# Kernel tuning notes

Hardware: AMD Instinct MI355X
Metric: run time of the kernel (lower is better)

The kernel has to match this reference:

```python
import jax, jax.numpy as jnp
import numpy as np

R = 29          # GF_kernel_size_train
EPS = 1e-09     # loss_eps
SAMPLING = 8    # sampling_in_MSEloss
LAMBDA_TV = 0.1
LAMBDA_HESSIAN = 0.5
ISO = True      # isotropic_hessian
SIGMA = 1.0     # hessian_kernel_sigma (>0.5 -> generateHessianKernel, angle_offset=[0])


def _hessian_kernels():
    half = int(np.ceil(SIGMA * 6))
    t = np.linspace(-half, half, 2 * half + 1)
    X, Y = np.meshgrid(t, t, indexing='ij')
    g = np.exp(-(X ** 2 + Y ** 2) / (2 * SIGMA ** 2))
    dxx = (1.0 / (2 * np.pi * SIGMA ** 4)) * (X ** 2 / SIGMA ** 2 - 1) * g
    dxy = (1.0 / (2 * np.pi * SIGMA ** 6)) * (X * Y) * g
    dyy = dxx.T
    # Loss.__init__ unpacks generateHessianKernel's return (Gaussyy, Gaussxx, Gaussxy)
    # into (self.DGaussxx, self.DGaussyy, self.DGaussxy); angle_offset=[0] -> identity rotate.
    Gxx = dyy.astype(np.float32)[None, None]
    Gyy = dxx.astype(np.float32)[None, None]
    Gxy = dxy.astype(np.float32)[None, None]
    return jnp.asarray(Gxx), jnp.asarray(Gyy), jnp.asarray(Gxy)


def _conv(x, k):
    return jax.lax.conv_general_dilated(x, k, (1, 1), 'VALID',
                                        dimension_numbers=('NCHW', 'OIHW', 'NCHW'))


def _boxfilter(x, r):
    # F.pad(input, (r+1, r, r+1, r)) pads last two dims (left r+1, right r each)
    xp = jnp.pad(x, ((0, 0), (0, 0), (r + 1, r), (r + 1, r)))
    c = jnp.cumsum(xp, axis=3)
    d = c[:, :, :, 2 * r + 1:] - c[:, :, :, :-2 * r - 1]
    c2 = jnp.cumsum(d, axis=2)
    return c2[:, :, 2 * r + 1:, :] - c2[:, :, :-2 * r - 1, :]


def _guided_filter(x, y, r, eps):
    N = _boxfilter(jnp.ones_like(x), r)
    mean_x = _boxfilter(x, r) / N
    mean_y = _boxfilter(y, r) / N
    cov_xy = _boxfilter(x * y, r) / N - mean_x * mean_y
    var_x = _boxfilter(x * x, r) / N - mean_x * mean_x
    A = cov_xy / jnp.clip(var_x, EPS, None)
    b = mean_y - A * mean_x
    A = _boxfilter(A, r) / N
    b = _boxfilter(b, r) / N
    return A * x + b


def _tv(x, target, Dx, Dy):
    return jnp.abs(_conv(x, Dx)).sum() + jnp.abs(_conv(x - target, Dy)).sum()


def _hessian(x, target, Gxx, Gyy, Gxy):
    scale = 2.0 if ISO else 1.0
    return (jnp.abs(_conv(x, Gxx)).sum()
            + jnp.abs(_conv(x - target, Gyy)).sum()
            + (jnp.abs(_conv(x - target, Gxy)) * scale).sum())


def setup_inputs() -> dict:
    key = jax.random.key(0)
    ks = jax.random.split(key, 6)
    shape = (1, 1, 3072, 3072)
    Gxx, Gyy, Gxy = _hessian_kernels()
    return {
        'outputGNNraw': jax.random.normal(ks[0], shape, dtype=jnp.float32),
        'outputGNN': jax.random.normal(ks[1], shape, dtype=jnp.float32),
        'outputLR': jax.random.normal(ks[2], shape, dtype=jnp.float32),
        'smoothedTarget': jax.random.normal(ks[3], shape, dtype=jnp.float32),
        'targets': jax.random.normal(ks[4], shape, dtype=jnp.float32),
        'map': jax.random.uniform(ks[5], shape, dtype=jnp.float32),
        'Dx': jnp.array([[1.0, -1.0]], dtype=jnp.float32)[None, None],   # [1,1,1,2]
        'Dy': jnp.array([[1.0], [-1.0]], dtype=jnp.float32)[None, None], # [1,1,2,1]
        'DGaussxx': Gxx, 'DGaussyy': Gyy, 'DGaussxy': Gxy,
    }


def reference(outputGNNraw, outputGNN, outputLR, smoothedTarget, targets, map,
              Dx, Dy, DGaussxx, DGaussyy, DGaussxy):
    gf = _guided_filter(outputGNNraw, outputGNNraw, R, EPS)
    mse = (jnp.abs(smoothedTarget - gf).sum()
           + (jnp.abs(targets - outputGNN) * map)[:, :, ::SAMPLING, ::SAMPLING].sum())
    tv = _tv(outputGNN, targets, Dx, Dy) + _tv(outputLR, targets, Dx, Dy)
    hess = (_hessian(outputGNN, targets, DGaussxx, DGaussyy, DGaussxy)
            + _hessian(outputLR, targets, DGaussxx, DGaussyy, DGaussxy))
    return mse + LAMBDA_TV * tv + LAMBDA_HESSIAN * hess
```

## Files before the change

### kernel.cpp

```cpp
#include <hip/hip_runtime.h>
#include <math.h>

#define W    3072
#define HH   3072
#define HOUT 3060
#define TW   64
#define TH   44
#define RW   11
#define XR   56
#define XTS  76
#define VTS  77
#define VTW  (RW*VTS)
#define GX   48
#define GY   70
#define GZ   2
#define NBLK (GX*GY*GZ)
#define NTHR (NBLK*256)
#define NSLOT 64
#define NSTG ((XR*19+255)/256)

struct HessTaps { float a[13]; float bb[13]; float m[13]; float n[13]; };

__device__ double g_slots[NSLOT * 32];

__global__ __launch_bounds__(256, 5) void hess_kernel(const float* __restrict__ Gnn,
                                                      const float* __restrict__ Lr,
                                                      const float* __restrict__ T,
                                                      const float* __restrict__ Xr,
                                                      const float* __restrict__ St,
                                                      const float* __restrict__ Mp,
                                                      HessTaps tp) {
  __shared__ float xt[XR * XTS];
  __shared__ float vt[4 * VTW];
  __shared__ float red[4][3];
  const float* img = (blockIdx.z == 0) ? Gnn : Lr;
  int oy = blockIdx.y * TH, ox = blockIdx.x * TW;
  int t = threadIdx.x;
  int wv = t >> 6, ln = t & 63;
  int r0 = wv * RW;

  for (int idx = t; idx < XR * 19; idx += 256) {
    int r = idx / 19, g = idx - r * 19;
    int gr = oy + r, gc = ox + 4 * g;
    float4 v = {0.f, 0.f, 0.f, 0.f};
    if (gr < HH) {
      const float* p = &img[(size_t)gr * W + gc];
      if (gc + 3 < W) v = *(const float4*)p;
      else {
        if (gc < W)     v.x = p[0];
        if (gc + 1 < W) v.y = p[1];
        if (gc + 2 < W) v.z = p[2];
      }
    }
    *(float4*)&xt[r * XTS + 4 * g] = v;
  }

  float4 tr4[NSTG];
  #pragma unroll
  for (int k = 0; k < NSTG; ++k) {
    int idx = t + 256 * k;
    float4 v = {0.f, 0.f, 0.f, 0.f};
    if (idx < XR * 19) {
      int r = idx / 19, g = idx - r * 19;
      int gr = oy + r, gc = ox + 4 * g;
      if (gr < HH) {
        const float* p = &T[(size_t)gr * W + gc];
        if (gc + 3 < W) v = *(const float4*)p;
        else {
          if (gc < W)     v.x = p[0];
          if (gc + 1 < W) v.y = p[1];
          if (gc + 2 < W) v.z = p[2];
        }
      }
    }
    tr4[k] = v;
  }

  int bid = (blockIdx.z * GY + blockIdx.y) * GX + blockIdx.x;
  int i0 = bid * 256 + t;
  int i1 = i0 + NTHR;
  const int n4 = (W * HH) / 4;
  float4 ga0 = ((const float4*)Xr)[i0];
  float4 gb0 = ((const float4*)St)[i0];
  float4 ga1 = {0.f, 0.f, 0.f, 0.f}, gb1 = ga1;
  bool has1 = (i1 < n4);
  if (has1) { ga1 = ((const float4*)Xr)[i1]; gb1 = ((const float4*)St)[i1]; }
  float mT = 0.f, mG = 0.f, mM = 0.f;
  bool hasm = (i0 < 384 * 384);
  if (hasm) {
    int si = i0 / 384, sj = i0 - si * 384;
    int id = si * 8 * W + sj * 8;
    mT = T[id]; mG = Gnn[id]; mM = Mp[id];
  }
  __builtin_amdgcn_sched_barrier(0);

  __syncthreads();

  float tvl = 0.f;
  float hl  = 0.f;

  {
    int gc = ox + ln;
    if (gc < W - 1) {
      #pragma unroll
      for (int i = 0; i < RW; ++i) {
        int r = r0 + i;
        if (oy + r < HH)
          tvl += fabsf(xt[r * XTS + ln] - xt[r * XTS + ln + 1]);
      }
    }
  }

  #define VPASS(TAP)                                                        \
    {                                                                       \
       \
      float oA[RW];                                                         \
      _Pragma("unroll")                                                     \
      for (int i = 0; i < RW; ++i) oA[i] = 0.f;                             \
      _Pragma("unroll")                                                     \
      for (int u = 0; u < RW + 12; ++u) {                                   \
        float xA = xt[(r0 + u) * XTS + ln];                                 \
        _Pragma("unroll")                                                   \
        for (int i = 0; i < RW; ++i) {                                      \
          int kk = u - i;                                                   \
          if (kk >= 0 && kk <= 12) oA[i] = fmaf((TAP)[kk], xA, oA[i]);      \
        }                                                                   \
      }                                                                     \
      float* vw = &vt[wv * VTW + ln];                                       \
      _Pragma("unroll")                                                     \
      for (int i = 0; i < RW; ++i) vw[i * VTS] = oA[i];                     \
                   \
      _Pragma("unroll")                                                     \
      for (int k = 0; k < 3; ++k) {                                         \
        int o = ln + 64 * k;                                                \
        if (o < 12 * RW) {                                                  \
          int row = o / 12, hc = o - row * 12;                              \
          const float* xp = &xt[(r0 + row) * XTS + 64 + hc];                \
          float s = 0.f;                                                    \
          _Pragma("unroll")                                                 \
          for (int u = 0; u < 13; ++u) s = fmaf((TAP)[u], xp[u * XTS], s);  \
          vt[wv * VTW + row * VTS + 64 + hc] = s;                           \
        }                                                                   \
      }                                                                     \
    }

  #define HSECOND(TAP, WGT)                                                 \
    {                                                                       \
      int r14 = ln & 15, cg = ln >> 4;                                      \
      if (r14 < RW) {                                                       \
        const float* vrow = &vt[wv * VTW + r14 * VTS + cg * 16];            \
        float o_[16];                                                       \
        _Pragma("unroll")                                                   \
        for (int jj = 0; jj < 16; ++jj) o_[jj] = 0.f;                       \
        _Pragma("unroll")                                                   \
        for (int j = 0; j < 28; ++j) {                                      \
          float v = vrow[j];                                                \
          _Pragma("unroll")                                                 \
          for (int jj = 0; jj < 16; ++jj) {                                 \
            int kk = j - jj;                                                \
            if (kk >= 0 && kk <= 12) o_[jj] = fmaf((TAP)[kk], v, o_[jj]);   \
          }                                                                 \
        }                                                                   \
        int gr = oy + r0 + r14;                                             \
        int gc0 = ox + cg * 16;                                             \
        float wr = (gr < HOUT) ? (WGT) : 0.f;                               \
        _Pragma("unroll")                                                   \
        for (int jj = 0; jj < 16; ++jj) {                                   \
          float m_ = (gc0 + jj < HOUT) ? wr : 0.f;                          \
          hl = fmaf(m_, fabsf(o_[jj]), hl);                                 \
        }                                                                   \
      }                                                                     \
    }

  VPASS(tp.bb);
  HSECOND(tp.a, 1.0f);

  __syncthreads();
  #pragma unroll
  for (int k = 0; k < NSTG; ++k) {
    int idx = t + 256 * k;
    if (idx < XR * 19) {
      int r = idx / 19, g = idx - r * 19;
      float4 cur = *(float4*)&xt[r * XTS + 4 * g];
      cur.x -= tr4[k].x; cur.y -= tr4[k].y;
      cur.z -= tr4[k].z; cur.w -= tr4[k].w;
      *(float4*)&xt[r * XTS + 4 * g] = cur;
    }
  }
  __syncthreads();

  {
    int gc = ox + ln;
    if (gc < W) {
      #pragma unroll
      for (int i = 0; i < RW; ++i) {
        int r = r0 + i;
        if (oy + r < HH - 1)
          tvl += fabsf(xt[r * XTS + ln] - xt[(r + 1) * XTS + ln]);
      }
    }
  }

  VPASS(tp.a);
  HSECOND(tp.bb, 1.0f);

  VPASS(tp.m);
  HSECOND(tp.n, 2.0f);

  float gm = fabsf(gb0.x - ga0.x) + fabsf(gb0.y - ga0.y)
           + fabsf(gb0.z - ga0.z) + fabsf(gb0.w - ga0.w);
  if (has1)
    gm += fabsf(gb1.x - ga1.x) + fabsf(gb1.y - ga1.y)
        + fabsf(gb1.z - ga1.z) + fabsf(gb1.w - ga1.w);
  if (hasm) gm += fabsf(mT - mG) * mM;

  #pragma unroll
  for (int o = 32; o > 0; o >>= 1) {
    gm  += __shfl_down(gm,  o, 64);
    tvl += __shfl_down(tvl, o, 64);
    hl  += __shfl_down(hl,  o, 64);
  }
  if (ln == 0) { red[wv][0] = gm; red[wv][1] = tvl; red[wv][2] = hl; }
  __syncthreads();
  if (t == 0) {
    int slot = bid & (NSLOT - 1);
    double* base = g_slots + (size_t)slot * 32;
    unsafeAtomicAdd(base,      (double)(red[0][0] + red[1][0] + red[2][0] + red[3][0]));
    unsafeAtomicAdd(base + 8,  (double)(red[0][1] + red[1][1] + red[2][1] + red[3][1]));
    unsafeAtomicAdd(base + 16, (double)(red[0][2] + red[1][2] + red[2][2] + red[3][2]));
  }
}

__global__ __launch_bounds__(64) void finalize_kernel(float* __restrict__ out) {
  int t = threadIdx.x;
  double* b = g_slots + (size_t)t * 32;
  double s0 = b[0];  b[0]  = 0.0;
  double s1 = b[8];  b[8]  = 0.0;
  double s3 = b[16]; b[16] = 0.0;
  #pragma unroll
  for (int o = 32; o > 0; o >>= 1) {
    s0 += __shfl_down(s0, o, 64);
    s1 += __shfl_down(s1, o, 64);
    s3 += __shfl_down(s3, o, 64);
  }
  if (t == 0) out[0] = (float)(s0 + 0.1 * s1 + 0.5 * s3);
}

extern "C" void kernel_launch(void* const* d_in, const int* in_sizes, int n_in,
                              void* d_out, int out_size, void* d_ws, size_t ws_size,
                              hipStream_t stream) {
  const float* xraw = (const float*)d_in[0];
  const float* gnn  = (const float*)d_in[1];
  const float* lr   = (const float*)d_in[2];
  const float* st   = (const float*)d_in[3];
  const float* tg   = (const float*)d_in[4];
  const float* mp   = (const float*)d_in[5];
  float* out = (float*)d_out;

  HessTaps tp;
  const double PI2 = 6.283185307179586476925287;
  for (int k = 0; k < 13; ++k) {
    double tt = (double)(k - 6);
    double g = exp(-0.5 * tt * tt);
    tp.a[k]  = (float)((tt * tt - 1.0) * g / PI2);
    tp.bb[k] = (float)g;
    tp.m[k]  = (float)(tt * g / PI2);
    tp.n[k]  = (float)(tt * g);
  }

  hess_kernel<<<dim3(GX, GY, GZ), 256, 0, stream>>>(gnn, lr, tg, xraw, st, mp,
                                                    tp);
  finalize_kernel<<<1, 64, 0, stream>>>(out);
}
```

Before: 260.1 us.

## Retile hessian kernel to 512-thread blocks with taller tiles and smaller per-wave strips

Moves to 8 waves per block, each handling 7 rows, with a 56-row tile to cut vertical halo redundancy. The horizontal second pass is remapped to 8-column segments per lane, and the MSE stream now needs only one float4 per thread. The trade-off is idle lanes in the horizontal pass and a tight launch bound that may cause register spills.

```diff
diff --git a/kernel.cpp b/kernel.cpp
--- a/kernel.cpp
+++ b/kernel.cpp
@@ -5,25 +5,26 @@
 #define HH   3072
 #define HOUT 3060
 #define TW   64
-#define TH   44
-#define RW   11
-#define XR   56
+#define TH   56
+#define RW   7
+#define NW   8
+#define XR   68
 #define XTS  76
 #define VTS  77
 #define VTW  (RW*VTS)
 #define GX   48
-#define GY   70
+#define GY   55
 #define GZ   2
 #define NBLK (GX*GY*GZ)
-#define NTHR (NBLK*256)
+#define NTHR (NBLK*512)
 #define NSLOT 64
-#define NSTG ((XR*19+255)/256)
+#define NSTG ((XR*19+511)/512)
 
 struct HessTaps { float a[13]; float bb[13]; float m[13]; float n[13]; };
 
 __device__ double g_slots[NSLOT * 32];
 
-__global__ __launch_bounds__(256, 5) void hess_kernel(const float* __restrict__ Gnn,
+__global__ __launch_bounds__(512, 8) void hess_kernel(const float* __restrict__ Gnn,
                                                       const float* __restrict__ Lr,
                                                       const float* __restrict__ T,
                                                       const float* __restrict__ Xr,
@@ -31,15 +32,15 @@
                                                       const float* __restrict__ Mp,
                                                       HessTaps tp) {
   __shared__ float xt[XR * XTS];
-  __shared__ float vt[4 * VTW];
-  __shared__ float red[4][3];
+  __shared__ float vt[NW * VTW];
+  __shared__ float red[NW][3];
   const float* img = (blockIdx.z == 0) ? Gnn : Lr;
   int oy = blockIdx.y * TH, ox = blockIdx.x * TW;
   int t = threadIdx.x;
   int wv = t >> 6, ln = t & 63;
   int r0 = wv * RW;
 
-  for (int idx = t; idx < XR * 19; idx += 256) {
+  for (int idx = t; idx < XR * 19; idx += 512) {
     int r = idx / 19, g = idx - r * 19;
     int gr = oy + r, gc = ox + 4 * g;
     float4 v = {0.f, 0.f, 0.f, 0.f};
@@ -58,7 +59,7 @@
   float4 tr4[NSTG];
   #pragma unroll
   for (int k = 0; k < NSTG; ++k) {
-    int idx = t + 256 * k;
+    int idx = t + 512 * k;
     float4 v = {0.f, 0.f, 0.f, 0.f};
     if (idx < XR * 19) {
       int r = idx / 19, g = idx - r * 19;
@@ -77,14 +78,11 @@
   }
 
   int bid = (blockIdx.z * GY + blockIdx.y) * GX + blockIdx.x;
-  int i0 = bid * 256 + t;
-  int i1 = i0 + NTHR;
+  int i0 = bid * 512 + t;
   const int n4 = (W * HH) / 4;
-  float4 ga0 = ((const float4*)Xr)[i0];
-  float4 gb0 = ((const float4*)St)[i0];
-  float4 ga1 = {0.f, 0.f, 0.f, 0.f}, gb1 = ga1;
-  bool has1 = (i1 < n4);
-  if (has1) { ga1 = ((const float4*)Xr)[i1]; gb1 = ((const float4*)St)[i1]; }
+  float4 ga0 = {0.f, 0.f, 0.f, 0.f}, gb0 = ga0;
+  bool has0 = (i0 < n4);
+  if (has0) { ga0 = ((const float4*)Xr)[i0]; gb0 = ((const float4*)St)[i0]; }
   float mT = 0.f, mG = 0.f, mM = 0.f;
   bool hasm = (i0 < 384 * 384);
   if (hasm) {
@@ -113,7 +111,7 @@
 
   #define VPASS(TAP)                                                        \
     {                                                                       \
-       \
+        \
       float oA[RW];                                                         \
       _Pragma("unroll")                                                     \
       for (int i = 0; i < RW; ++i) oA[i] = 0.f;                             \
@@ -129,9 +127,9 @@
       float* vw = &vt[wv * VTW + ln];                                       \
       _Pragma("unroll")                                                     \
       for (int i = 0; i < RW; ++i) vw[i * VTS] = oA[i];                     \
-                   \
-      _Pragma("unroll")                                                     \
-      for (int k = 0; k < 3; ++k) {                                         \
+                     \
+      _Pragma("unroll")                                                     \
+      for (int k = 0; k < 2; ++k) {                                         \
         int o = ln + 64 * k;                                                \
         if (o < 12 * RW) {                                                  \
           int row = o / 12, hc = o - row * 12;                              \
@@ -146,26 +144,26 @@
 
   #define HSECOND(TAP, WGT)                                                 \
     {                                                                       \
-      int r14 = ln & 15, cg = ln >> 4;                                      \
-      if (r14 < RW) {                                                       \
-        const float* vrow = &vt[wv * VTW + r14 * VTS + cg * 16];            \
-        float o_[16];                                                       \
-        _Pragma("unroll")                                                   \
-        for (int jj = 0; jj < 16; ++jj) o_[jj] = 0.f;                       \
-        _Pragma("unroll")                                                   \
-        for (int j = 0; j < 28; ++j) {                                      \
+      int r8 = ln >> 3, cg = ln & 7;                                        \
+      if (r8 < RW) {                                                        \
+        const float* vrow = &vt[wv * VTW + r8 * VTS + cg * 8];              \
+        float o_[8];                                                        \
+        _Pragma("unroll")                                                   \
+        for (int jj = 0; jj < 8; ++jj) o_[jj] = 0.f;                        \
+        _Pragma("unroll")                                                   \
+        for (int j = 0; j < 20; ++j) {                                      \
           float v = vrow[j];                                                \
           _Pragma("unroll")                                                 \
-          for (int jj = 0; jj < 16; ++jj) {                                 \
+          for (int jj = 0; jj < 8; ++jj) {                                  \
             int kk = j - jj;                                                \
             if (kk >= 0 && kk <= 12) o_[jj] = fmaf((TAP)[kk], v, o_[jj]);   \
           }                                                                 \
         }                                                                   \
-        int gr = oy + r0 + r14;                                             \
-        int gc0 = ox + cg * 16;                                             \
+        int gr = oy + r0 + r8;                                              \
+        int gc0 = ox + cg * 8;                                              \
         float wr = (gr < HOUT) ? (WGT) : 0.f;                               \
         _Pragma("unroll")                                                   \
-        for (int jj = 0; jj < 16; ++jj) {                                   \
+        for (int jj = 0; jj < 8; ++jj) {                                    \
           float m_ = (gc0 + jj < HOUT) ? wr : 0.f;                          \
           hl = fmaf(m_, fabsf(o_[jj]), hl);                                 \
         }                                                                   \
@@ -178,7 +176,7 @@
   __syncthreads();
   #pragma unroll
   for (int k = 0; k < NSTG; ++k) {
-    int idx = t + 256 * k;
+    int idx = t + 512 * k;
     if (idx < XR * 19) {
       int r = idx / 19, g = idx - r * 19;
       float4 cur = *(float4*)&xt[r * XTS + 4 * g];
@@ -207,11 +205,10 @@
   VPASS(tp.m);
   HSECOND(tp.n, 2.0f);
 
-  float gm = fabsf(gb0.x - ga0.x) + fabsf(gb0.y - ga0.y)
-           + fabsf(gb0.z - ga0.z) + fabsf(gb0.w - ga0.w);
-  if (has1)
-    gm += fabsf(gb1.x - ga1.x) + fabsf(gb1.y - ga1.y)
-        + fabsf(gb1.z - ga1.z) + fabsf(gb1.w - ga1.w);
+  float gm = 0.f;
+  if (has0)
+    gm = fabsf(gb0.x - ga0.x) + fabsf(gb0.y - ga0.y)
+       + fabsf(gb0.z - ga0.z) + fabsf(gb0.w - ga0.w);
   if (hasm) gm += fabsf(mT - mG) * mM;
 
   #pragma unroll
@@ -223,11 +220,16 @@
   if (ln == 0) { red[wv][0] = gm; red[wv][1] = tvl; red[wv][2] = hl; }
   __syncthreads();
   if (t == 0) {
+    float s0 = 0.f, s1 = 0.f, s2 = 0.f;
+    #pragma unroll
+    for (int w = 0; w < NW; ++w) {
+      s0 += red[w][0]; s1 += red[w][1]; s2 += red[w][2];
+    }
     int slot = bid & (NSLOT - 1);
     double* base = g_slots + (size_t)slot * 32;
-    unsafeAtomicAdd(base,      (double)(red[0][0] + red[1][0] + red[2][0] + red[3][0]));
-    unsafeAtomicAdd(base + 8,  (double)(red[0][1] + red[1][1] + red[2][1] + red[3][1]));
-    unsafeAtomicAdd(base + 16, (double)(red[0][2] + red[1][2] + red[2][2] + red[3][2]));
+    unsafeAtomicAdd(base,      (double)s0);
+    unsafeAtomicAdd(base + 8,  (double)s1);
+    unsafeAtomicAdd(base + 16, (double)s2);
   }
 }
 
@@ -268,7 +270,7 @@
     tp.n[k]  = (float)(tt * g);
   }
 
-  hess_kernel<<<dim3(GX, GY, GZ), 256, 0, stream>>>(gnn, lr, tg, xraw, st, mp,
+  hess_kernel<<<dim3(GX, GY, GZ), 512, 0, stream>>>(gnn, lr, tg, xraw, st, mp,
                                                     tp);
   finalize_kernel<<<1, 64, 0, stream>>>(out);
 }
```

After: 251.2 us. 1.04x faster.
